# Kernel optimization log

Measured on AMD Instinct MI355X. Metric: run time of the kernel, lower is better.

## Reference

```python
import jax, jax.numpy as jnp
import numpy as np

EMBED = 128
NUM_HOPS = 3
VOCAB = 32000
MEM = 50
PAD = 0


def pos_weights(J, d):
    # MemN2N position encoding: 1 - (j+1)/J - (k+1)/d * (1 - 2*(j+1)/J)
    j = jnp.arange(J, dtype=jnp.float32)[:, None]
    k = jnp.arange(d, dtype=jnp.float32)[None, :]
    return 1.0 - (j + 1.0) / J - (k + 1.0) / d * (1.0 - 2.0 * (j + 1.0) / J)


def setup_inputs() -> dict:
    key = jax.random.key(0)
    ks = jax.random.split(key, 10)
    ctx_query = jax.random.randint(ks[0], (16, 10, 20), 0, VOCAB)
    story = jax.random.randint(ks[1], (16, MEM, 40), 0, VOCAB)

    def emb(k):
        w = 0.1 * jax.random.normal(k, (VOCAB, EMBED), dtype=jnp.float32)
        return w.at[PAD].set(0.0)  # padding_idx row is zero

    A_w = emb(ks[2])
    C_w = emb(ks[3])
    B_w = emb(ks[4])
    H_w = 0.1 * jax.random.normal(ks[5], (EMBED, EMBED), dtype=jnp.float32)
    H_b = 0.1 * jax.random.normal(ks[6], (EMBED,), dtype=jnp.float32)
    out_w = 0.1 * jax.random.normal(ks[7], (VOCAB, EMBED), dtype=jnp.float32)
    TA = 0.1 * jax.random.normal(ks[8], (MEM, EMBED), dtype=jnp.float32)
    TC = 0.1 * jax.random.normal(ks[9], (MEM, EMBED), dtype=jnp.float32)
    return {"ctx_query": ctx_query, "story": story, "A_w": A_w, "C_w": C_w,
            "B_w": B_w, "H_w": H_w, "H_b": H_b, "out_w": out_w, "TA": TA, "TC": TC}


def reference(ctx_query, story, A_w, C_w, B_w, H_w, H_b, out_w, TA, TC):
    B, NQ, S = ctx_query.shape
    R, S2 = story.shape[1], story.shape[2]
    cq = ctx_query.reshape(B * NQ, S)
    # story repeated across num_qa (broadcast instead of materialized repeat)
    st = jnp.broadcast_to(story[:, None], (B, NQ, R, S2)).reshape(B * NQ, R, S2)

    qw = pos_weights(S, EMBED)            # [S, d]
    state = jnp.sum(B_w[cq] * qw, axis=1)  # [BN, d]

    sw = pos_weights(S2, EMBED)           # [S2, d]
    for _ in range(NUM_HOPS):             # use_lw=True: A/C tied across hops
        mem = jnp.sum(A_w[st] * sw, axis=2) + TA    # [BN, R, d]
        outm = jnp.sum(C_w[st] * sw, axis=2) + TC   # [BN, R, d]
        probs = jax.nn.softmax(jnp.einsum('brd,bd->br', mem, state), axis=-1)
        response = jnp.einsum('br,brd->bd', probs, outm)  # [BN, d]
        state = response @ H_w.T + H_b + state      # H(response) + state
    return state @ out_w.T                          # [BN, vocab]
```

## Files before the change

kernel.cpp:

```cpp
#include <hip/hip_runtime.h>
#include <hip/hip_bf16.h>
#include <math.h>

#define EMBED 128
#define VOCAB 32000
#define MEMN  50
#define BATCH 16
#define NQ    10
#define SQ    20
#define SS    40
#define BN    (BATCH*NQ)
#define NHOPS 3
#define NV    64

typedef short v8s __attribute__((ext_vector_type(8)));
typedef float v4f __attribute__((ext_vector_type(4)));

#define MFMA16 __builtin_amdgcn_mfma_f32_16x16x32_bf16

__device__ __forceinline__ float posw(int j, int J, int k) {
    float jf = (float)(j + 1) / (float)J;
    return 1.0f - jf - ((float)(k + 1) / (float)EMBED) * (1.0f - 2.0f * jf);
}

__device__ __forceinline__ short f2bf(float f) {
    __hip_bfloat16 h = __float2bfloat16(f);
    return *(short*)&h;
}
__device__ __forceinline__ float bf2f(short s) {
    __hip_bfloat16 h = *(__hip_bfloat16*)&s;
    return __bfloat162float(h);
}

__global__ void k_embed(const int* __restrict__ cq, const int* __restrict__ story,
                        const float* __restrict__ Bw, const float* __restrict__ Aw,
                        const float* __restrict__ Cw, const float* __restrict__ TA,
                        const float* __restrict__ TC, const float* __restrict__ Hw,
                        float* __restrict__ state, float* __restrict__ memb,
                        float* __restrict__ outb, short* __restrict__ HwBhi,
                        short* __restrict__ HwBlo) {
    int blk = blockIdx.x;
    int t = threadIdx.x;
    if (blk < BN) {
        float acc = 0.f;
        #pragma unroll
        for (int s = 0; s < SQ; ++s) {
            int tok = cq[blk * SQ + s];
            acc += Bw[tok * EMBED + t] * posw(s, SQ, t);
        }
        state[blk * EMBED + t] = acc;
    } else if (blk < BN + BATCH * MEMN) {
        int br = blk - BN;
        int r = br % MEMN;
        float ma = TA[r * EMBED + t];
        float mc = TC[r * EMBED + t];
        const int* toks = story + br * SS;
        #pragma unroll 4
        for (int s = 0; s < SS; ++s) {
            int tok = toks[s];
            float w = posw(s, SS, t);
            ma += Aw[tok * EMBED + t] * w;
            mc += Cw[tok * EMBED + t] * w;
        }
        memb[br * EMBED + t] = ma;
        outb[br * EMBED + t] = mc;
    } else {
        int row = blk - (BN + BATCH * MEMN);
        float v = Hw[row * EMBED + t];
        short h = f2bf(v);
        HwBhi[row * EMBED + t] = h;
        HwBlo[row * EMBED + t] = f2bf(v - bf2f(h));
    }
}

__global__ __launch_bounds__(256) void k_hops(const float* __restrict__ memb,
                                              const float* __restrict__ outb,
                                              const short* __restrict__ HwBhi,
                                              const short* __restrict__ HwBlo,
                                              const float* __restrict__ Hb,
                                              const float* __restrict__ state,
                                              __hip_bfloat16* __restrict__ stateb) {
    __shared__ short mem_hi[64][128], mem_lo[64][128];
    __shared__ short outT_hi[128][64], outT_lo[128][64];
    __shared__ short P_hi[16][64], P_lo[16][64];
    __shared__ short resp_hi[16][128], resp_lo[16][128];
    __shared__ float stateM[16][132];
    __shared__ float Lg[16][64];
    __shared__ float Hb_l[128];

    int b = blockIdx.x;
    int t = threadIdx.x;
    int w = t >> 6;
    int l = t & 63;
    int c16 = l & 15;
    int kg = l >> 4;

    {
        v8s z = {0,0,0,0,0,0,0,0};
        for (int i = t; i < 64*128/8; i += 256) { ((v8s*)mem_hi)[i] = z; ((v8s*)mem_lo)[i] = z; }
        for (int i = t; i < 128*64/8; i += 256) { ((v8s*)outT_hi)[i] = z; ((v8s*)outT_lo)[i] = z; }
        for (int i = t; i < 16*64/8;  i += 256) { ((v8s*)P_hi)[i] = z; ((v8s*)P_lo)[i] = z; }
        for (int i = t; i < 16*132;   i += 256) ((float*)stateM)[i] = 0.f;
    }
    __syncthreads();

    {
        const float4* mb4 = (const float4*)(memb + (size_t)b * MEMN * EMBED);
        const float4* ob4 = (const float4*)(outb + (size_t)b * MEMN * EMBED);
        for (int i = t; i < MEMN * EMBED / 4; i += 256) {
            int r = i >> 5, c4 = (i & 31) << 2;
            float4 v = mb4[i];
            float4 u = ob4[i];
            float mv[4] = {v.x, v.y, v.z, v.w};
            float ov[4] = {u.x, u.y, u.z, u.w};
            #pragma unroll
            for (int j = 0; j < 4; ++j) {
                int k = c4 + j;
                short h = f2bf(mv[j]);
                int pos = (((k >> 3) ^ (r & 15)) << 3) | (k & 7);
                mem_hi[r][pos] = h;
                mem_lo[r][pos] = f2bf(mv[j] - bf2f(h));
                short g = f2bf(ov[j]);
                int posT = (((r >> 3) ^ (k & 7)) << 3) | (r & 7);
                outT_hi[k][posT] = g;
                outT_lo[k][posT] = f2bf(ov[j] - bf2f(g));
            }
        }
        for (int i = t; i < NQ * EMBED; i += 256) {
            int q = i >> 7, d = i & 127;
            stateM[q][d] = state[((size_t)b * NQ + q) * EMBED + d];
        }
        if (t < 128) Hb_l[t] = Hb[t];
    }
    __syncthreads();

    for (int hop = 0; hop < NHOPS; ++hop) {
        {
            v4f acc = {0.f, 0.f, 0.f, 0.f};
            int mrow = (w << 4) + c16;
            #pragma unroll
            for (int ks = 0; ks < 4; ++ks) {
                float4 s0 = *(const float4*)&stateM[c16][ks*32 + kg*8];
                float4 s1 = *(const float4*)&stateM[c16][ks*32 + kg*8 + 4];
                float sv[8] = {s0.x, s0.y, s0.z, s0.w, s1.x, s1.y, s1.z, s1.w};
                v8s ah, al;
                #pragma unroll
                for (int j = 0; j < 8; ++j) {
                    short h = f2bf(sv[j]);
                    ah[j] = h;
                    al[j] = f2bf(sv[j] - bf2f(h));
                }
                int pos = ((ks*4 + kg) ^ (mrow & 15)) << 3;
                v8s bh = *(const v8s*)&mem_hi[mrow][pos];
                v8s bl = *(const v8s*)&mem_lo[mrow][pos];
                acc = MFMA16(ah, bh, acc, 0, 0, 0);
                acc = MFMA16(al, bh, acc, 0, 0, 0);
                acc = MFMA16(ah, bl, acc, 0, 0, 0);
            }
            #pragma unroll
            for (int i = 0; i < 4; ++i) Lg[kg*4 + i][(w << 4) + c16] = acc[i];
        }
        __syncthreads();
        for (int q = w; q < NQ; q += 4) {
            float v = (l < MEMN) ? Lg[q][l] : -1e30f;
            float mx = v;
            #pragma unroll
            for (int off = 32; off; off >>= 1) mx = fmaxf(mx, __shfl_xor(mx, off, 64));
            float e = (l < MEMN) ? __expf(v - mx) : 0.f;
            float ss = e;
            #pragma unroll
            for (int off = 32; off; off >>= 1) ss += __shfl_xor(ss, off, 64);
            if (l < MEMN) {
                float p = e / ss;
                short h = f2bf(p);
                int pos = (((l >> 3) ^ (q & 7)) << 3) | (l & 7);
                P_hi[q][pos] = h;
                P_lo[q][pos] = f2bf(p - bf2f(h));
            }
        }
        __syncthreads();
        {
            v8s ph[2], pl[2];
            #pragma unroll
            for (int ks = 0; ks < 2; ++ks) {
                int pos = ((ks*4 + kg) ^ (c16 & 7)) << 3;
                ph[ks] = *(const v8s*)&P_hi[c16][pos];
                pl[ks] = *(const v8s*)&P_lo[c16][pos];
            }
            #pragma unroll
            for (int tile = 0; tile < 2; ++tile) {
                int d = (w << 4) + tile * 64;
                int orow = d + c16;
                v4f acc = {0.f, 0.f, 0.f, 0.f};
                #pragma unroll
                for (int ks = 0; ks < 2; ++ks) {
                    int pos = ((ks*4 + kg) ^ (orow & 7)) << 3;
                    v8s bh = *(const v8s*)&outT_hi[orow][pos];
                    v8s bl = *(const v8s*)&outT_lo[orow][pos];
                    acc = MFMA16(ph[ks], bh, acc, 0, 0, 0);
                    acc = MFMA16(pl[ks], bh, acc, 0, 0, 0);
                    acc = MFMA16(ph[ks], bl, acc, 0, 0, 0);
                }
                #pragma unroll
                for (int i = 0; i < 4; ++i) {
                    int row = kg*4 + i, col = d + c16;
                    float v = acc[i];
                    short h = f2bf(v);
                    int pos = (((col >> 3) ^ (row & 15)) << 3) | (col & 7);
                    resp_hi[row][pos] = h;
                    resp_lo[row][pos] = f2bf(v - bf2f(h));
                }
            }
        }
        __syncthreads();
        {
            v8s rh[4], rl[4];
            #pragma unroll
            for (int ks = 0; ks < 4; ++ks) {
                int pos = ((ks*4 + kg) ^ (c16 & 15)) << 3;
                rh[ks] = *(const v8s*)&resp_hi[c16][pos];
                rl[ks] = *(const v8s*)&resp_lo[c16][pos];
            }
            #pragma unroll
            for (int tile = 0; tile < 2; ++tile) {
                int d = (w << 4) + tile * 64;
                int hrow = d + c16;
                const v8s* gh = (const v8s*)(HwBhi + (size_t)hrow * EMBED);
                const v8s* gl = (const v8s*)(HwBlo + (size_t)hrow * EMBED);
                v4f acc = {0.f, 0.f, 0.f, 0.f};
                #pragma unroll
                for (int ks = 0; ks < 4; ++ks) {
                    v8s bh = gh[ks*4 + kg];
                    v8s bl = gl[ks*4 + kg];
                    acc = MFMA16(rh[ks], bh, acc, 0, 0, 0);
                    acc = MFMA16(rl[ks], bh, acc, 0, 0, 0);
                    acc = MFMA16(rh[ks], bl, acc, 0, 0, 0);
                }
                #pragma unroll
                for (int i = 0; i < 4; ++i) {
                    int row = kg*4 + i, col = d + c16;
                    stateM[row][col] = acc[i] + Hb_l[col] + stateM[row][col];
                }
            }
        }
        __syncthreads();
    }
    for (int i = t; i < NQ * EMBED; i += 256) {
        int q = i >> 7, d = i & 127;
        stateb[((size_t)b * NQ + q) * EMBED + d] = __float2bfloat16(stateM[q][d]);
    }
}

__global__ __launch_bounds__(256) void k_out(const __hip_bfloat16* __restrict__ stateb,
                                             const float* __restrict__ outw,
                                             float* __restrict__ out) {
    __shared__ __align__(16) __hip_bfloat16 Alds[BN][EMBED + 8];
    __shared__ __align__(16) __hip_bfloat16 Blds[NV][EMBED + 8];
    int t = threadIdx.x;
    int vbase = blockIdx.x * NV;

    #pragma unroll
    for (int i = 0; i < 10; ++i) {
        int e = t + i * 256;
        int row = e >> 4, c8 = (e & 15) << 3;
        *(int4*)&Alds[row][c8] = *(const int4*)&stateb[row * EMBED + c8];
    }
    #pragma unroll
    for (int i = 0; i < 8; ++i) {
        int e = t + i * 256;
        int row = e >> 5, c4 = (e & 31) << 2;
        float4 w = *(const float4*)&outw[(size_t)(vbase + row) * EMBED + c4];
        short4 p;
        p.x = f2bf(w.x); p.y = f2bf(w.y); p.z = f2bf(w.z); p.w = f2bf(w.w);
        *(short4*)&Blds[row][c4] = p;
    }
    __syncthreads();

    int wv = t >> 6;
    int l = t & 63;
    int col16 = l & 15;
    int kg = l >> 4;

    v8s bfrag[4];
    #pragma unroll
    for (int k4 = 0; k4 < 4; ++k4)
        bfrag[k4] = *(v8s*)&Blds[(wv << 4) + col16][k4 * 32 + kg * 8];

    v4f acc[10];
    #pragma unroll
    for (int m = 0; m < 10; ++m) acc[m] = (v4f){0.f, 0.f, 0.f, 0.f};

    #pragma unroll
    for (int k4 = 0; k4 < 4; ++k4) {
        #pragma unroll
        for (int m = 0; m < 10; ++m) {
            v8s af = *(v8s*)&Alds[m * 16 + col16][k4 * 32 + kg * 8];
            acc[m] = MFMA16(af, bfrag[k4], acc[m], 0, 0, 0);
        }
    }

    int colg = vbase + (wv << 4) + col16;
    #pragma unroll
    for (int m = 0; m < 10; ++m) {
        #pragma unroll
        for (int i = 0; i < 4; ++i) {
            out[(size_t)(m * 16 + kg * 4 + i) * VOCAB + colg] = acc[m][i];
        }
    }
}

extern "C" void kernel_launch(void* const* d_in, const int* in_sizes, int n_in,
                              void* d_out, int out_size, void* d_ws, size_t ws_size,
                              hipStream_t stream) {
    const int*   ctx_query = (const int*)  d_in[0];
    const int*   story     = (const int*)  d_in[1];
    const float* A_w       = (const float*)d_in[2];
    const float* C_w       = (const float*)d_in[3];
    const float* B_w       = (const float*)d_in[4];
    const float* H_w       = (const float*)d_in[5];
    const float* H_b       = (const float*)d_in[6];
    const float* out_w     = (const float*)d_in[7];
    const float* TA        = (const float*)d_in[8];
    const float* TC        = (const float*)d_in[9];
    float* out = (float*)d_out;

    float* ws    = (float*)d_ws;
    float* state = ws;
    float* memb  = state + BN * EMBED;
    float* outb  = memb + BATCH * MEMN * EMBED;
    short* HwBhi = (short*)(outb + BATCH * MEMN * EMBED);
    short* HwBlo = HwBhi + EMBED * EMBED;
    __hip_bfloat16* stateb = (__hip_bfloat16*)(HwBlo + EMBED * EMBED);

    k_embed<<<BN + BATCH * MEMN + EMBED, 128, 0, stream>>>(
        ctx_query, story, B_w, A_w, C_w, TA, TC, H_w, state, memb, outb, HwBhi, HwBlo);
    k_hops<<<BATCH, 256, 0, stream>>>(memb, outb, HwBhi, HwBlo, H_b, state, stateb);
    k_out<<<VOCAB / NV, 256, 0, stream>>>(stateb, out_w, out);
}
```

Baseline: 36.89 us.

## Precompute memory-hop Gram matrices so hops update logits without per-hop GEMMs

Uses the linearity of the hop recurrence to precompute OH = outm·Hᵀ and G = mem·OHᵀ once per batch, plus mem·Hb. Each hop then updates the logits directly with lg += mem·Hb + G·p inside a single wave, with no block-wide barriers. The final state is formed as state0 + 3·Hb + (sum of probs)·OH. The goal is to remove the serialized per-hop MFMA stages and the __syncthreads between them. The cost is extra upfront GEMM work and different rounding, because the products are reassociated in split-bf16.

```diff
diff --git a/kernel.cpp b/kernel.cpp
--- a/kernel.cpp
+++ b/kernel.cpp
@@ -30,6 +30,17 @@
 __device__ __forceinline__ float bf2f(short s) {
     __hip_bfloat16 h = *(__hip_bfloat16*)&s;
     return __bfloat162float(h);
+}
+
+__device__ __forceinline__ float wave_softmax(float v, int l) {
+    float mx = v;
+    #pragma unroll
+    for (int off = 32; off; off >>= 1) mx = fmaxf(mx, __shfl_xor(mx, off, 64));
+    float e = (l < MEMN) ? __expf(v - mx) : 0.f;
+    float ss = e;
+    #pragma unroll
+    for (int off = 32; off; off >>= 1) ss += __shfl_xor(ss, off, 64);
+    return e / ss;
 }
 
 __global__ void k_embed(const int* __restrict__ cq, const int* __restrict__ story,
@@ -81,12 +92,12 @@
                                               const float* __restrict__ state,
                                               __hip_bfloat16* __restrict__ stateb) {
     __shared__ short mem_hi[64][128], mem_lo[64][128];
-    __shared__ short outT_hi[128][64], outT_lo[128][64];
-    __shared__ short P_hi[16][64], P_lo[16][64];
-    __shared__ short resp_hi[16][128], resp_lo[16][128];
+    __shared__ short out_hi[64][128], out_lo[64][128];
+    __shared__ short OH_hi[64][128], OH_lo[64][128];
+    __shared__ float G[64][65];
     __shared__ float stateM[16][132];
-    __shared__ float Lg[16][64];
-    __shared__ float Hb_l[128];
+    __shared__ float Lg[16][65];
+    __shared__ float Ps[16][53];
 
     int b = blockIdx.x;
     int t = threadIdx.x;
@@ -96,158 +107,196 @@
     int kg = l >> 4;
 
     {
-        v8s z = {0,0,0,0,0,0,0,0};
-        for (int i = t; i < 64*128/8; i += 256) { ((v8s*)mem_hi)[i] = z; ((v8s*)mem_lo)[i] = z; }
-        for (int i = t; i < 128*64/8; i += 256) { ((v8s*)outT_hi)[i] = z; ((v8s*)outT_lo)[i] = z; }
-        for (int i = t; i < 16*64/8;  i += 256) { ((v8s*)P_hi)[i] = z; ((v8s*)P_lo)[i] = z; }
-        for (int i = t; i < 16*132;   i += 256) ((float*)stateM)[i] = 0.f;
-    }
-    __syncthreads();
-
-    {
-        const float4* mb4 = (const float4*)(memb + (size_t)b * MEMN * EMBED);
-        const float4* ob4 = (const float4*)(outb + (size_t)b * MEMN * EMBED);
-        for (int i = t; i < MEMN * EMBED / 4; i += 256) {
-            int r = i >> 5, c4 = (i & 31) << 2;
-            float4 v = mb4[i];
-            float4 u = ob4[i];
-            float mv[4] = {v.x, v.y, v.z, v.w};
-            float ov[4] = {u.x, u.y, u.z, u.w};
-            #pragma unroll
-            for (int j = 0; j < 4; ++j) {
-                int k = c4 + j;
-                short h = f2bf(mv[j]);
-                int pos = (((k >> 3) ^ (r & 15)) << 3) | (k & 7);
-                mem_hi[r][pos] = h;
-                mem_lo[r][pos] = f2bf(mv[j] - bf2f(h));
-                short g = f2bf(ov[j]);
-                int posT = (((r >> 3) ^ (k & 7)) << 3) | (r & 7);
-                outT_hi[k][posT] = g;
-                outT_lo[k][posT] = f2bf(ov[j] - bf2f(g));
-            }
-        }
-        for (int i = t; i < NQ * EMBED; i += 256) {
-            int q = i >> 7, d = i & 127;
-            stateM[q][d] = state[((size_t)b * NQ + q) * EMBED + d];
-        }
-        if (t < 128) Hb_l[t] = Hb[t];
-    }
-    __syncthreads();
-
-    for (int hop = 0; hop < NHOPS; ++hop) {
+        const float* mb = memb + (size_t)b * MEMN * EMBED;
+        const float* ob = outb + (size_t)b * MEMN * EMBED;
+        for (int i = t; i < MEMN * 16; i += 256) {
+            int r = i >> 4, c8 = i & 15;
+            const float4* m4 = (const float4*)&mb[r * EMBED + (c8 << 3)];
+            const float4* o4 = (const float4*)&ob[r * EMBED + (c8 << 3)];
+            float4 v0 = m4[0], v1 = m4[1], u0 = o4[0], u1 = o4[1];
+            float mv[8] = {v0.x,v0.y,v0.z,v0.w,v1.x,v1.y,v1.z,v1.w};
+            float ov[8] = {u0.x,u0.y,u0.z,u0.w,u1.x,u1.y,u1.z,u1.w};
+            v8s mh, ml, oh, ol;
+            #pragma unroll
+            for (int j = 0; j < 8; ++j) {
+                short h = f2bf(mv[j]); mh[j] = h; ml[j] = f2bf(mv[j] - bf2f(h));
+                short g = f2bf(ov[j]); oh[j] = g; ol[j] = f2bf(ov[j] - bf2f(g));
+            }
+            int pos = (c8 ^ (r & 15)) << 3;
+            *(v8s*)&mem_hi[r][pos] = mh;
+            *(v8s*)&mem_lo[r][pos] = ml;
+            *(v8s*)&out_hi[r][pos] = oh;
+            *(v8s*)&out_lo[r][pos] = ol;
+        }
+        for (int i = t; i < 14 * 16; i += 256) {
+            int r = 50 + (i >> 4), c8 = i & 15;
+            v8s z = {0,0,0,0,0,0,0,0};
+            int pos = (c8 ^ (r & 15)) << 3;
+            *(v8s*)&mem_hi[r][pos] = z;
+            *(v8s*)&mem_lo[r][pos] = z;
+            *(v8s*)&out_hi[r][pos] = z;
+            *(v8s*)&out_lo[r][pos] = z;
+        }
+        for (int i = t; i < 16 * 132; i += 256) {
+            int q = i / 132, d = i - q * 132;
+            float v = 0.f;
+            if (d < EMBED) {
+                if (q < NQ) v = state[((size_t)b * NQ + q) * EMBED + d];
+                else if (q == NQ) v = Hb[d];
+            }
+            (&stateM[0][0])[i] = v;
+        }
+    }
+    __syncthreads();
+
+    {
+        int stile = w;
+        v8s ah[4], al[4];
+        #pragma unroll
+        for (int ks = 0; ks < 4; ++ks) {
+            int arow = (stile << 4) + c16;
+            int pos = (((ks * 4 + kg) ^ (arow & 15)) << 3);
+            ah[ks] = *(const v8s*)&out_hi[arow][pos];
+            al[ks] = *(const v8s*)&out_lo[arow][pos];
+        }
+        #pragma unroll
+        for (int dt = 0; dt < 8; ++dt) {
+            int brow = (dt << 4) + c16;
+            const v8s* gh = (const v8s*)(HwBhi + (size_t)brow * EMBED);
+            const v8s* gl = (const v8s*)(HwBlo + (size_t)brow * EMBED);
+            v4f A1 = {0,0,0,0}, A2 = {0,0,0,0}, A3 = {0,0,0,0};
+            #pragma unroll
+            for (int ks = 0; ks < 4; ++ks) {
+                v8s bh = gh[ks * 4 + kg], bl = gl[ks * 4 + kg];
+                A1 = MFMA16(ah[ks], bh, A1, 0, 0, 0);
+                A2 = MFMA16(al[ks], bh, A2, 0, 0, 0);
+                A3 = MFMA16(ah[ks], bl, A3, 0, 0, 0);
+            }
+            #pragma unroll
+            for (int e = 0; e < 4; ++e) {
+                int s = (stile << 4) + kg * 4 + e;
+                int d = (dt << 4) + c16;
+                float v = A1[e] + A2[e] + A3[e];
+                short h = f2bf(v);
+                int pp = (((d >> 3) ^ (s & 15)) << 3) | (d & 7);
+                OH_hi[s][pp] = h;
+                OH_lo[s][pp] = f2bf(v - bf2f(h));
+            }
+        }
         {
-            v4f acc = {0.f, 0.f, 0.f, 0.f};
-            int mrow = (w << 4) + c16;
+            int brow = (w << 4) + c16;
+            v4f A1 = {0,0,0,0}, A2 = {0,0,0,0}, A3 = {0,0,0,0};
             #pragma unroll
             for (int ks = 0; ks < 4; ++ks) {
-                float4 s0 = *(const float4*)&stateM[c16][ks*32 + kg*8];
-                float4 s1 = *(const float4*)&stateM[c16][ks*32 + kg*8 + 4];
-                float sv[8] = {s0.x, s0.y, s0.z, s0.w, s1.x, s1.y, s1.z, s1.w};
-                v8s ah, al;
+                float4 s0 = *(const float4*)&stateM[c16][ks * 32 + kg * 8];
+                float4 s1 = *(const float4*)&stateM[c16][ks * 32 + kg * 8 + 4];
+                float sv[8] = {s0.x,s0.y,s0.z,s0.w,s1.x,s1.y,s1.z,s1.w};
+                v8s sh, sl;
                 #pragma unroll
                 for (int j = 0; j < 8; ++j) {
-                    short h = f2bf(sv[j]);
-                    ah[j] = h;
-                    al[j] = f2bf(sv[j] - bf2f(h));
+                    short h = f2bf(sv[j]); sh[j] = h; sl[j] = f2bf(sv[j] - bf2f(h));
                 }
-                int pos = ((ks*4 + kg) ^ (mrow & 15)) << 3;
-                v8s bh = *(const v8s*)&mem_hi[mrow][pos];
-                v8s bl = *(const v8s*)&mem_lo[mrow][pos];
-                acc = MFMA16(ah, bh, acc, 0, 0, 0);
-                acc = MFMA16(al, bh, acc, 0, 0, 0);
-                acc = MFMA16(ah, bl, acc, 0, 0, 0);
-            }
-            #pragma unroll
-            for (int i = 0; i < 4; ++i) Lg[kg*4 + i][(w << 4) + c16] = acc[i];
-        }
-        __syncthreads();
-        for (int q = w; q < NQ; q += 4) {
-            float v = (l < MEMN) ? Lg[q][l] : -1e30f;
-            float mx = v;
-            #pragma unroll
-            for (int off = 32; off; off >>= 1) mx = fmaxf(mx, __shfl_xor(mx, off, 64));
-            float e = (l < MEMN) ? __expf(v - mx) : 0.f;
-            float ss = e;
-            #pragma unroll
-            for (int off = 32; off; off >>= 1) ss += __shfl_xor(ss, off, 64);
+                int pos = (((ks * 4 + kg) ^ (brow & 15)) << 3);
+                v8s bh = *(const v8s*)&mem_hi[brow][pos];
+                v8s bl = *(const v8s*)&mem_lo[brow][pos];
+                A1 = MFMA16(sh, bh, A1, 0, 0, 0);
+                A2 = MFMA16(sl, bh, A2, 0, 0, 0);
+                A3 = MFMA16(sh, bl, A3, 0, 0, 0);
+            }
+            #pragma unroll
+            for (int e = 0; e < 4; ++e)
+                Lg[kg * 4 + e][(w << 4) + c16] = A1[e] + A2[e] + A3[e];
+        }
+    }
+    __syncthreads();
+
+    {
+        int rtile = w;
+        v8s ah[4], al[4];
+        #pragma unroll
+        for (int ks = 0; ks < 4; ++ks) {
+            int arow = (rtile << 4) + c16;
+            int pos = (((ks * 4 + kg) ^ (arow & 15)) << 3);
+            ah[ks] = *(const v8s*)&mem_hi[arow][pos];
+            al[ks] = *(const v8s*)&mem_lo[arow][pos];
+        }
+        #pragma unroll
+        for (int st = 0; st < 4; ++st) {
+            int brow = (st << 4) + c16;
+            v4f A1 = {0,0,0,0}, A2 = {0,0,0,0}, A3 = {0,0,0,0};
+            #pragma unroll
+            for (int ks = 0; ks < 4; ++ks) {
+                int pos = (((ks * 4 + kg) ^ (brow & 15)) << 3);
+                v8s bh = *(const v8s*)&OH_hi[brow][pos];
+                v8s bl = *(const v8s*)&OH_lo[brow][pos];
+                A1 = MFMA16(ah[ks], bh, A1, 0, 0, 0);
+                A2 = MFMA16(al[ks], bh, A2, 0, 0, 0);
+                A3 = MFMA16(ah[ks], bl, A3, 0, 0, 0);
+            }
+            #pragma unroll
+            for (int e = 0; e < 4; ++e)
+                G[(rtile << 4) + kg * 4 + e][(st << 4) + c16] = A1[e] + A2[e] + A3[e];
+        }
+    }
+    __syncthreads();
+
+    {
+        float lg0 = (l < MEMN) ? Lg[w][l] : -1e30f;
+        float lg1 = (l < MEMN) ? Lg[w + 4][l] : -1e30f;
+        float lg2 = (l < MEMN && w < 2) ? Lg[w + 8][l] : -1e30f;
+        float mhb = (l < MEMN) ? Lg[NQ][l] : 0.f;
+        float ps0 = 0.f, ps1 = 0.f, ps2 = 0.f;
+        #pragma unroll
+        for (int hop = 0; hop < NHOPS; ++hop) {
+            float p0 = wave_softmax(lg0, l);
+            float p1 = wave_softmax(lg1, l);
+            float p2 = wave_softmax(lg2, l);
+            ps0 += p0; ps1 += p1; ps2 += p2;
+            if (hop == NHOPS - 1) break;
             if (l < MEMN) {
-                float p = e / ss;
-                short h = f2bf(p);
-                int pos = (((l >> 3) ^ (q & 7)) << 3) | (l & 7);
-                P_hi[q][pos] = h;
-                P_lo[q][pos] = f2bf(p - bf2f(h));
-            }
-        }
-        __syncthreads();
-        {
-            v8s ph[2], pl[2];
-            #pragma unroll
-            for (int ks = 0; ks < 2; ++ks) {
-                int pos = ((ks*4 + kg) ^ (c16 & 7)) << 3;
-                ph[ks] = *(const v8s*)&P_hi[c16][pos];
-                pl[ks] = *(const v8s*)&P_lo[c16][pos];
-            }
-            #pragma unroll
-            for (int tile = 0; tile < 2; ++tile) {
-                int d = (w << 4) + tile * 64;
-                int orow = d + c16;
-                v4f acc = {0.f, 0.f, 0.f, 0.f};
-                #pragma unroll
-                for (int ks = 0; ks < 2; ++ks) {
-                    int pos = ((ks*4 + kg) ^ (orow & 7)) << 3;
-                    v8s bh = *(const v8s*)&outT_hi[orow][pos];
-                    v8s bl = *(const v8s*)&outT_lo[orow][pos];
-                    acc = MFMA16(ph[ks], bh, acc, 0, 0, 0);
-                    acc = MFMA16(pl[ks], bh, acc, 0, 0, 0);
-                    acc = MFMA16(ph[ks], bl, acc, 0, 0, 0);
-                }
-                #pragma unroll
-                for (int i = 0; i < 4; ++i) {
-                    int row = kg*4 + i, col = d + c16;
-                    float v = acc[i];
-                    short h = f2bf(v);
-                    int pos = (((col >> 3) ^ (row & 15)) << 3) | (col & 7);
-                    resp_hi[row][pos] = h;
-                    resp_lo[row][pos] = f2bf(v - bf2f(h));
-                }
-            }
-        }
-        __syncthreads();
-        {
-            v8s rh[4], rl[4];
-            #pragma unroll
-            for (int ks = 0; ks < 4; ++ks) {
-                int pos = ((ks*4 + kg) ^ (c16 & 15)) << 3;
-                rh[ks] = *(const v8s*)&resp_hi[c16][pos];
-                rl[ks] = *(const v8s*)&resp_lo[c16][pos];
-            }
-            #pragma unroll
-            for (int tile = 0; tile < 2; ++tile) {
-                int d = (w << 4) + tile * 64;
-                int hrow = d + c16;
-                const v8s* gh = (const v8s*)(HwBhi + (size_t)hrow * EMBED);
-                const v8s* gl = (const v8s*)(HwBlo + (size_t)hrow * EMBED);
-                v4f acc = {0.f, 0.f, 0.f, 0.f};
-                #pragma unroll
-                for (int ks = 0; ks < 4; ++ks) {
-                    v8s bh = gh[ks*4 + kg];
-                    v8s bl = gl[ks*4 + kg];
-                    acc = MFMA16(rh[ks], bh, acc, 0, 0, 0);
-                    acc = MFMA16(rl[ks], bh, acc, 0, 0, 0);
-                    acc = MFMA16(rh[ks], bl, acc, 0, 0, 0);
-                }
-                #pragma unroll
-                for (int i = 0; i < 4; ++i) {
-                    int row = kg*4 + i, col = d + c16;
-                    stateM[row][col] = acc[i] + Hb_l[col] + stateM[row][col];
-                }
-            }
-        }
-        __syncthreads();
-    }
-    for (int i = t; i < NQ * EMBED; i += 256) {
-        int q = i >> 7, d = i & 127;
-        stateb[((size_t)b * NQ + q) * EMBED + d] = __float2bfloat16(stateM[q][d]);
+                Ps[w][l] = p0;
+                Ps[w + 4][l] = p1;
+                if (w < 2) Ps[w + 8][l] = p2;
+            }
+            asm volatile("" ::: "memory");
+            float a0 = 0.f, a1 = 0.f, a2 = 0.f;
+            float b0 = 0.f, b1 = 0.f, b2 = 0.f;
+            for (int s = 0; s < MEMN; s += 2) {
+                float g0 = G[l][s], g1 = G[l][s + 1];
+                a0 += g0 * Ps[w][s];      b0 += g1 * Ps[w][s + 1];
+                a1 += g0 * Ps[w + 4][s];  b1 += g1 * Ps[w + 4][s + 1];
+                if (w < 2) { a2 += g0 * Ps[w + 8][s]; b2 += g1 * Ps[w + 8][s + 1]; }
+            }
+            lg0 += mhb + (a0 + b0);
+            lg1 += mhb + (a1 + b1);
+            lg2 += mhb + (a2 + b2);
+        }
+        if (l < MEMN) {
+            Ps[w][l] = ps0;
+            Ps[w + 4][l] = ps1;
+            if (w < 2) Ps[w + 8][l] = ps2;
+        }
+    }
+    __syncthreads();
+
+    {
+        int d = t & 127;
+        int qb = t >> 7;
+        float acc[5] = {0.f, 0.f, 0.f, 0.f, 0.f};
+        for (int s = 0; s < MEMN; ++s) {
+            int pp = (((d >> 3) ^ (s & 15)) << 3) | (d & 7);
+            float ov = bf2f(OH_hi[s][pp]) + bf2f(OH_lo[s][pp]);
+            #pragma unroll
+            for (int j = 0; j < 5; ++j)
+                acc[j] += Ps[qb + j * 2][s] * ov;
+        }
+        float hb3 = 3.f * stateM[NQ][d];
+        #pragma unroll
+        for (int j = 0; j < 5; ++j) {
+            int q = qb + j * 2;
+            stateb[((size_t)b * NQ + q) * EMBED + d] =
+                __float2bfloat16(stateM[q][d] + hb3 + acc[j]);
+        }
     }
 }
 
```

New measurement: 42.28 us. +14.6%, slower.
